# Optimization experiments

Hardware: AMD Instinct MI355X
Metric: run time of the kernel (lower is better)

## Reference

```python
import jax, jax.numpy as jnp
import numpy as np


def setup_inputs() -> dict:
    key = jax.random.key(0)
    k1, k2 = jax.random.split(key)
    B, T_src, H = 32, 1024, 512
    x = jax.random.normal(k1, (B, T_src, H), dtype=jnp.float32)
    durations = jax.random.randint(k2, (B, T_src), 0, 8, dtype=jnp.int32)
    return {"x": x, "durations": durations}


def reference(x, durations):
    """Length regulator: repeat each source frame x[b, s] durations[b, s] times,
    pad batch to the max expanded length, return (expanded, mel_masks) where
    mel_masks is True at padded positions. Vectorized via cumulative-duration
    searchsorted gather instead of per-batch repeat_interleave.
    x: (B, T_src, H) float, durations: (B, T_src) int.
    """
    B, T_src, H = x.shape
    cum = jnp.cumsum(durations.astype(jnp.int32), axis=1)      # (B, T_src)
    totals = cum[:, -1]                                        # (B,)
    max_len = int(jnp.max(totals))                             # static: concrete inputs
    t = jnp.arange(max_len, dtype=jnp.int32)                   # (T_mel,)
    # src index of output frame t: first s with cum[b, s] > t
    idx = jax.vmap(lambda c: jnp.searchsorted(c, t, side='right'))(cum)  # (B, T_mel)
    idx = jnp.clip(idx, 0, T_src - 1)
    out = jnp.take_along_axis(x, idx[..., None], axis=1)       # (B, T_mel, H)
    mel_masks = t[None, :] >= totals[:, None]                  # (B, T_mel) True = pad
    out = jnp.where(mel_masks[..., None], jnp.zeros((), dtype=x.dtype), out)
    return out, mel_masks
```

## Files before the change

### kernel.cpp

```cpp
#include <hip/hip_runtime.h>


#define B_SZ   32
#define T_SRC  1024
#define H_DIM  512

__global__ void __launch_bounds__(T_SRC) lr_prep(const int* __restrict__ dur,
                                                 int* __restrict__ idxbuf,
                                                 float* __restrict__ mask,
                                                 int max_len) {
    __shared__ int s[T_SRC];
    const int b   = blockIdx.x;
    const int tid = threadIdx.x;
    s[tid] = dur[b * T_SRC + tid];
    __syncthreads();
#pragma unroll
    for (int off = 1; off < T_SRC; off <<= 1) {
        int v = (tid >= off) ? s[tid - off] : 0;
        __syncthreads();
        s[tid] += v;
        __syncthreads();
    }
    const int end   = s[tid];
    const int start = tid ? s[tid - 1] : 0;
    const int total = s[T_SRC - 1];

    int* ib = idxbuf + (size_t)b * max_len;
    for (int t = start; t < end; ++t) ib[t] = tid;
    for (int t = total + tid; t < max_len; t += T_SRC) ib[t] = -1;
    float* mb = mask + (size_t)b * max_len;
    for (int t = tid; t < max_len; t += T_SRC) mb[t] = (t < total) ? 0.0f : 1.0f;
}

__global__ void __launch_bounds__(256) lr_copy(const float* __restrict__ x,
                                               const int* __restrict__ idxbuf,
                                               float* __restrict__ out,
                                               int max_len, int nwaves_x) {
    const int b    = blockIdx.y;
    const int lane = threadIdx.x & 63;
    const int wv   = (blockIdx.x << 2) | (threadIdx.x >> 6);

    const int*   ib = idxbuf + (size_t)b * max_len;
    const float* xb = x      + (size_t)b * T_SRC   * H_DIM;
    float*       ob = out    + (size_t)b * max_len * H_DIM;

    for (int t = wv; t < max_len; t += nwaves_x) {
        const int sidx = ib[t];
        float4 v0 = make_float4(0.f, 0.f, 0.f, 0.f), v1 = v0;
        if (sidx >= 0) {
            const float4* src = (const float4*)(xb + (size_t)sidx * H_DIM);
            v0 = src[lane];
            v1 = src[lane + 64];
        }
        float4* dst = (float4*)(ob + (size_t)t * H_DIM);
        dst[lane]      = v0;
        dst[lane + 64] = v1;
    }
}

extern "C" void kernel_launch(void* const* d_in, const int* in_sizes, int n_in,
                              void* d_out, int out_size, void* d_ws, size_t ws_size,
                              hipStream_t stream) {
    const float* x   = (const float*)d_in[0];
    const int*   dur = (const int*)d_in[1];
    float*       out = (float*)d_out;
    int*         idxbuf = (int*)d_ws;

    const int max_len = out_size / (B_SZ * (H_DIM + 1));
    float* mask = out + (size_t)B_SZ * max_len * H_DIM;

    lr_prep<<<B_SZ, T_SRC, 0, stream>>>(dur, idxbuf, mask, max_len);

    const int gx = 64;
    dim3 grid(gx, B_SZ);
    lr_copy<<<grid, 256, 0, stream>>>(x, idxbuf, out, max_len, gx * 4);
}
```

Measured before the change: 299.3 us.

## Scatter copy by source frame with nontemporal stores instead of per-output gather

The prep kernel now writes only the cumulative durations instead of expanding a per-output-frame index buffer. The copy kernel assigns one wave per source frame: it loads the frame once and writes it to all of its repeated output positions with nontemporal stores, and the waves also zero the padded tail. This removes the index buffer writes and reads and the repeated loads of the same source row, at the cost of load imbalance across waves when durations vary. The grid grows to one wave per source frame.

```diff
diff --git a/kernel.cpp b/kernel.cpp
--- a/kernel.cpp
+++ b/kernel.cpp
@@ -5,8 +5,10 @@
 #define T_SRC  1024
 #define H_DIM  512
 
+typedef float f4 __attribute__((ext_vector_type(4)));
+
 __global__ void __launch_bounds__(T_SRC) lr_prep(const int* __restrict__ dur,
-                                                 int* __restrict__ idxbuf,
+                                                 int* __restrict__ cum,
                                                  float* __restrict__ mask,
                                                  int max_len) {
     __shared__ int s[T_SRC];
@@ -21,40 +23,42 @@
         s[tid] += v;
         __syncthreads();
     }
-    const int end   = s[tid];
-    const int start = tid ? s[tid - 1] : 0;
+    cum[b * T_SRC + tid] = s[tid];
     const int total = s[T_SRC - 1];
-
-    int* ib = idxbuf + (size_t)b * max_len;
-    for (int t = start; t < end; ++t) ib[t] = tid;
-    for (int t = total + tid; t < max_len; t += T_SRC) ib[t] = -1;
     float* mb = mask + (size_t)b * max_len;
     for (int t = tid; t < max_len; t += T_SRC) mb[t] = (t < total) ? 0.0f : 1.0f;
 }
 
 __global__ void __launch_bounds__(256) lr_copy(const float* __restrict__ x,
-                                               const int* __restrict__ idxbuf,
+                                               const int* __restrict__ cum,
                                                float* __restrict__ out,
-                                               int max_len, int nwaves_x) {
+                                               int max_len) {
     const int b    = blockIdx.y;
     const int lane = threadIdx.x & 63;
-    const int wv   = (blockIdx.x << 2) | (threadIdx.x >> 6);
+    const int s    = (blockIdx.x << 2) | (threadIdx.x >> 6);
 
-    const int*   ib = idxbuf + (size_t)b * max_len;
-    const float* xb = x      + (size_t)b * T_SRC   * H_DIM;
-    float*       ob = out    + (size_t)b * max_len * H_DIM;
+    const int* cb = cum + b * T_SRC;
 
-    for (int t = wv; t < max_len; t += nwaves_x) {
-        const int sidx = ib[t];
-        float4 v0 = make_float4(0.f, 0.f, 0.f, 0.f), v1 = v0;
-        if (sidx >= 0) {
-            const float4* src = (const float4*)(xb + (size_t)sidx * H_DIM);
-            v0 = src[lane];
-            v1 = src[lane + 64];
-        }
-        float4* dst = (float4*)(ob + (size_t)t * H_DIM);
-        dst[lane]      = v0;
-        dst[lane + 64] = v1;
+    const f4* src = (const f4*)(x + ((size_t)b * T_SRC + s) * H_DIM);
+    const f4 v0 = src[lane];
+    const f4 v1 = src[lane + 64];
+
+    const int end   = cb[s];
+    const int start = s ? cb[s - 1] : 0;
+
+    float* ob = out + (size_t)b * max_len * H_DIM;
+    for (int t = start; t < end; ++t) {
+        f4* dst = (f4*)(ob + (size_t)t * H_DIM);
+        __builtin_nontemporal_store(v0, dst + lane);
+        __builtin_nontemporal_store(v1, dst + lane + 64);
+    }
+
+    const int total = cb[T_SRC - 1];
+    const f4 z = (f4)(0.0f);
+    for (int t = total + s; t < max_len; t += T_SRC) {
+        f4* dst = (f4*)(ob + (size_t)t * H_DIM);
+        __builtin_nontemporal_store(z, dst + lane);
+        __builtin_nontemporal_store(z, dst + lane + 64);
     }
 }
 
@@ -64,14 +68,13 @@
     const float* x   = (const float*)d_in[0];
     const int*   dur = (const int*)d_in[1];
     float*       out = (float*)d_out;
-    int*         idxbuf = (int*)d_ws;
+    int*         cumbuf = (int*)d_ws;
 
     const int max_len = out_size / (B_SZ * (H_DIM + 1));
     float* mask = out + (size_t)B_SZ * max_len * H_DIM;
 
-    lr_prep<<<B_SZ, T_SRC, 0, stream>>>(dur, idxbuf, mask, max_len);
+    lr_prep<<<B_SZ, T_SRC, 0, stream>>>(dur, cumbuf, mask, max_len);
 
-    const int gx = 64;
-    dim3 grid(gx, B_SZ);
-    lr_copy<<<grid, 256, 0, stream>>>(x, idxbuf, out, max_len, gx * 4);
+    dim3 grid(T_SRC / 4, B_SZ);
+    lr_copy<<<grid, 256, 0, stream>>>(x, cumbuf, out, max_len);
 }
```

Result: faster. 293.0 us (-2.1%).
